# Optimization experiments

Hardware: AMD Instinct MI355X
Metric: run time of the kernel (lower is better)

The kernel has to match this reference:

```python
import jax, jax.numpy as jnp
import numpy as np
from math import sqrt

KERNEL = 25
INV_SQRT2 = 1.0 / sqrt(2.0)


def _moving_avg(xt):
    # xt: [B, L]; replicate-pad then average-pool k=25 stride=1 -> [B, L]
    pad_l = (KERNEL - 1) // 2
    pad_r = KERNEL - 1 - pad_l
    xp = jnp.pad(xt, ((0, 0), (pad_l, pad_r)), mode='edge')[:, None, :]  # [B,1,Lp]
    k = jnp.full((1, 1, KERNEL), 1.0 / KERNEL, dtype=xt.dtype)  # [O,I,W]
    out = jax.lax.conv_general_dilated(xp, k, window_strides=(1,), padding='VALID',
                                       dimension_numbers=('NCH', 'OIH', 'NCH'))
    return out[:, 0, :]


def setup_inputs() -> dict:
    key = jax.random.key(0)
    ks = jax.random.split(key, 7)
    B, L, P, H = 8192, 4096, 720, 2048
    return {
        'x': jax.random.normal(ks[0], (B, L, 1), dtype=jnp.float32),
        'W_trend': jax.random.normal(ks[1], (P, L), dtype=jnp.float32) * 0.02,
        'b_trend': jax.random.normal(ks[2], (P,), dtype=jnp.float32) * 0.02,
        'W_lo': jax.random.normal(ks[3], (P, H), dtype=jnp.float32) * 0.02,
        'b_lo': jax.random.normal(ks[4], (P,), dtype=jnp.float32) * 0.02,
        'W_hi': jax.random.normal(ks[5], (P, H), dtype=jnp.float32) * 0.02,
        'b_hi': jax.random.normal(ks[6], (P,), dtype=jnp.float32) * 0.02,
    }


def reference(x, W_trend, b_trend, W_lo, b_lo, W_hi, b_hi):
    xt = x[..., 0]                              # [B, L]
    trend = _moving_avg(xt)                     # [B, L]
    res = xt - trend                            # [B, L]
    res_mean = jnp.mean(res, axis=-1, keepdims=True)
    # torch.std is unbiased (ddof=1)
    res_std = jnp.std(res, axis=-1, keepdims=True, ddof=1) + 1e-5
    res_norm = (res - res_mean) / res_std       # [B, L]
    # Haar DWT (stride-2 conv with [1,1]/sqrt2 and [1,-1]/sqrt2); L even -> no pad
    even, odd = res_norm[:, 0::2], res_norm[:, 1::2]  # [B, L/2]
    res_lo = (even + odd) * INV_SQRT2
    res_hi = (even - odd) * INV_SQRT2
    pred_trend = trend @ W_trend.T + b_trend    # [B, P]
    pred_res = (res_lo @ W_lo.T + b_lo) + (res_hi @ W_hi.T + b_hi)
    total = pred_trend + pred_res * res_std     # res_std broadcasts [B,1]
    return total[..., None]                     # [B, P, 1]
```

## Files before the change

kernel.cpp:

```cpp
#include <hip/hip_runtime.h>

typedef unsigned short u16;
typedef unsigned int   u32;
typedef __attribute__((ext_vector_type(8))) short bf16x8;
typedef __attribute__((ext_vector_type(4))) float f32x4;

#define LROW 4096
#define NB   8192
#define PCOL 720
#define NPAD 768
#define HH   2048
#define INV_SQRT2F 0.70710678118654752440f

#define WS_XBF_BYTES ((size_t)67108864)
#define WS_G_BYTES   ((size_t)6291456)
#define WS_MIN       (WS_XBF_BYTES + WS_G_BYTES + (size_t)NB * 4)

__device__ __forceinline__ u16 f2bf(float f) {
    union { float f; u32 u; } v; v.f = f;
    u32 r = v.u + 0x7FFFu + ((v.u >> 16) & 1u);
    return (u16)(r >> 16);
}

#define SWZ(i) ((i) ^ (((i) >> 5) & 31))

__global__ __launch_bounds__(256) void prep_rows(const float* __restrict__ x,
                                                 u16* __restrict__ xbf,
                                                 float* __restrict__ stdv) {
    __shared__ float S[LROW];
    __shared__ float wred[4];
    __shared__ float ends[2];
    __shared__ float rred[8];
    const int tid = threadIdx.x;
    const int lane = tid & 63, wv = tid >> 6;
    const size_t b = blockIdx.x;

    const float4* xr4 = (const float4*)(x + b * LROW);
    float4 q0 = xr4[tid * 4 + 0], q1 = xr4[tid * 4 + 1];
    float4 q2 = xr4[tid * 4 + 2], q3 = xr4[tid * 4 + 3];
    float r[16];
    r[0]=q0.x; r[1]=q0.y; r[2]=q0.z; r[3]=q0.w;
    r[4]=q1.x; r[5]=q1.y; r[6]=q1.z; r[7]=q1.w;
    r[8]=q2.x; r[9]=q2.y; r[10]=q2.z; r[11]=q2.w;
    r[12]=q3.x; r[13]=q3.y; r[14]=q3.z; r[15]=q3.w;

    float ps[16];
    float a = 0.f;
    #pragma unroll
    for (int k = 0; k < 16; ++k) { a += r[k]; ps[k] = a; }
    const float segsum = a;

    float v = segsum;
    #pragma unroll
    for (int off = 1; off < 64; off <<= 1) {
        float o = __shfl_up(v, off);
        if (lane >= off) v += o;
    }
    if (lane == 63) wred[wv] = v;
    if (tid == 0)   ends[0] = r[0];
    if (tid == 255) ends[1] = r[15];
    __syncthreads();

    float wbase = 0.f;
    #pragma unroll
    for (int w = 0; w < 4; ++w) if (w < wv) wbase += wred[w];
    const float ebase = wbase + v - segsum;

    #pragma unroll
    for (int k = 0; k < 16; ++k) {
        const int i = (tid << 4) + k;
        S[SWZ(i)] = ebase + ps[k];
    }
    __syncthreads();

    const float x0 = ends[0], xl = ends[1];
    float s1 = 0.f, s2 = 0.f;
    u16 ob[16];
    #pragma unroll
    for (int k = 0; k < 16; ++k) {
        const int i = (tid << 4) + k;
        int h = i + 12; h = h > LROW - 1 ? LROW - 1 : h;
        float wsum = S[SWZ(h)];
        if (i >= 13) wsum -= S[SWZ(i - 13)];
        if (i < 12) wsum += (float)(12 - i) * x0;
        if (i > LROW - 13) wsum += (float)(i - (LROW - 13)) * xl;
        const float xi = r[k];
        const float rr = xi - wsum * 0.04f;
        s1 += rr; s2 += rr * rr;
        ob[k] = f2bf(xi);
    }

    uint4 o0, o1;
    o0.x = (u32)ob[0]  | ((u32)ob[1]  << 16);
    o0.y = (u32)ob[2]  | ((u32)ob[3]  << 16);
    o0.z = (u32)ob[4]  | ((u32)ob[5]  << 16);
    o0.w = (u32)ob[6]  | ((u32)ob[7]  << 16);
    o1.x = (u32)ob[8]  | ((u32)ob[9]  << 16);
    o1.y = (u32)ob[10] | ((u32)ob[11] << 16);
    o1.z = (u32)ob[12] | ((u32)ob[13] << 16);
    o1.w = (u32)ob[14] | ((u32)ob[15] << 16);
    uint4* op = (uint4*)(xbf + b * LROW + ((size_t)tid << 4));
    op[0] = o0; op[1] = o1;

    #pragma unroll
    for (int off = 32; off; off >>= 1) {
        s1 += __shfl_down(s1, off);
        s2 += __shfl_down(s2, off);
    }
    if (lane == 0) { rred[wv * 2] = s1; rred[wv * 2 + 1] = s2; }
    __syncthreads();
    if (tid == 0) {
        const float S1 = rred[0] + rred[2] + rred[4] + rred[6];
        const float S2 = rred[1] + rred[3] + rred[5] + rred[7];
        const float mean = S1 / (float)LROW;
        float var = (S2 - (float)LROW * mean * mean) / (float)(LROW - 1);
        var = var < 0.f ? 0.f : var;
        stdv[b] = sqrtf(var) + 1e-5f;
    }
}

__global__ __launch_bounds__(256) void prep_weights(const float* __restrict__ Wt,
                                                    const float* __restrict__ Wlo,
                                                    const float* __restrict__ Whi,
                                                    u16* __restrict__ Gm) {
    __shared__ float S[LROW];
    __shared__ float wred[4];
    __shared__ float sred[4];
    const int tid = threadIdx.x;
    const int lane = tid & 63, wv = tid >> 6;
    const int p = blockIdx.x;
    u16* grow = Gm + (size_t)p * LROW;
    if (p >= PCOL) {
        uint4 z; z.x = z.y = z.z = z.w = 0u;
        uint4* g4 = (uint4*)grow;
        for (int i = tid; i < LROW / 8; i += 256) g4[i] = z;
        return;
    }
    const float4* wt4 = (const float4*)(Wt + (size_t)p * LROW);
    float4 q0 = wt4[tid * 4 + 0], q1 = wt4[tid * 4 + 1];
    float4 q2 = wt4[tid * 4 + 2], q3 = wt4[tid * 4 + 3];
    const float4* lo4 = (const float4*)(Wlo + (size_t)p * HH);
    const float4* hi4 = (const float4*)(Whi + (size_t)p * HH);
    float4 a0 = lo4[tid * 2 + 0], a1 = lo4[tid * 2 + 1];
    float4 b0 = hi4[tid * 2 + 0], b1 = hi4[tid * 2 + 1];

    float w[16];
    w[0]=q0.x; w[1]=q0.y; w[2]=q0.z; w[3]=q0.w;
    w[4]=q1.x; w[5]=q1.y; w[6]=q1.z; w[7]=q1.w;
    w[8]=q2.x; w[9]=q2.y; w[10]=q2.z; w[11]=q2.w;
    w[12]=q3.x; w[13]=q3.y; w[14]=q3.z; w[15]=q3.w;
    float lv[8] = {a0.x,a0.y,a0.z,a0.w,a1.x,a1.y,a1.z,a1.w};
    float hv[8] = {b0.x,b0.y,b0.z,b0.w,b1.x,b1.y,b1.z,b1.w};

    float u[16], z_[16];
    float slo = 0.f;
    #pragma unroll
    for (int j = 0; j < 8; ++j) {
        u[2*j]   = (lv[j] + hv[j]) * INV_SQRT2F;
        u[2*j+1] = (lv[j] - hv[j]) * INV_SQRT2F;
        slo += lv[j];
    }
    #pragma unroll
    for (int k = 0; k < 16; ++k) z_[k] = w[k] - u[k];

    float ps[16];
    float a = 0.f;
    #pragma unroll
    for (int k = 0; k < 16; ++k) { a += z_[k]; ps[k] = a; }
    const float segsum = a;

    float v = segsum;
    #pragma unroll
    for (int off = 1; off < 64; off <<= 1) {
        float o = __shfl_up(v, off);
        if (lane >= off) v += o;
    }
    if (lane == 63) wred[wv] = v;
    #pragma unroll
    for (int off = 32; off; off >>= 1) slo += __shfl_down(slo, off);
    if (lane == 0) sred[wv] = slo;
    __syncthreads();

    float wbase = 0.f;
    #pragma unroll
    for (int ww = 0; ww < 4; ++ww) if (ww < wv) wbase += wred[ww];
    const float ebase = wbase + v - segsum;
    const float SLO = sred[0] + sred[1] + sred[2] + sred[3];

    #pragma unroll
    for (int k = 0; k < 16; ++k) {
        const int i = (tid << 4) + k;
        S[SWZ(i)] = ebase + ps[k];
    }
    __syncthreads();

    const float coef = -1.4142135623730951f * SLO / (float)LROW;
    u16 ob[16];
    #pragma unroll
    for (int k = 0; k < 16; ++k) {
        const int l = (tid << 4) + k;
        float zT;
        if (l == 0) {
            float acc = 0.f;
            for (int m = 0; m <= 12; ++m) acc += S[SWZ(m)];
            zT = acc * 0.04f;
        } else if (l == LROW - 1) {
            float acc = 0.f;
            for (int m = 0; m <= 12; ++m) acc += S[SWZ(LROW - 2 - m)];
            zT = (13.f * S[SWZ(LROW - 1)] - acc) * 0.04f;
        } else {
            int h = l + 12; h = h > LROW - 1 ? LROW - 1 : h;
            float t_ = S[SWZ(h)];
            if (l >= 13) t_ -= S[SWZ(l - 13)];
            zT = t_ * 0.04f;
        }
        float c;
        const int dmin = l < (LROW - 1 - l) ? l : (LROW - 1 - l);
        if (dmin >= 12)      c = 0.f;
        else if (dmin == 0)  c = -66.f / 25.f;
        else                 c = (float)(12 - dmin) * 0.04f;
        ob[k] = f2bf(zT + u[k] + coef * c);
    }

    uint4 o0, o1;
    o0.x = (u32)ob[0]  | ((u32)ob[1]  << 16);
    o0.y = (u32)ob[2]  | ((u32)ob[3]  << 16);
    o0.z = (u32)ob[4]  | ((u32)ob[5]  << 16);
    o0.w = (u32)ob[6]  | ((u32)ob[7]  << 16);
    o1.x = (u32)ob[8]  | ((u32)ob[9]  << 16);
    o1.y = (u32)ob[10] | ((u32)ob[11] << 16);
    o1.z = (u32)ob[12] | ((u32)ob[13] << 16);
    o1.w = (u32)ob[14] | ((u32)ob[15] << 16);
    uint4* op = (uint4*)(grow + ((size_t)tid << 4));
    op[0] = o0; op[1] = o1;
}

typedef __attribute__((address_space(1))) void gvoid;
typedef __attribute__((address_space(3))) void lvoid;
#define GLD16(g, l_) __builtin_amdgcn_global_load_lds((gvoid*)(g), (lvoid*)(l_), 16, 0, 0)
#define MF(a, b, c) __builtin_amdgcn_mfma_f32_16x16x32_bf16(a, b, c, 0, 0, 0)

#define ABUF 16384
#define BBASE 49152
#define BBUF 12288

#define STAGE_A2(T, DB) do { \
    char* d_ = Sm + (DB) * ABUF; \
    const size_t go_ = (size_t)((T) + 2) * 128; \
    GLD16(s0 + go_, d_ + dof0); GLD16(s1 + go_, d_ + dof1); \
    GLD16(s2 + go_, d_ + dof2); GLD16(s3 + go_, d_ + dof3); \
} while (0)

#define STAGE_B1(T, DB) do { \
    char* d_ = Sm + BBASE + (DB) * BBUF; \
    const size_t go_ = (size_t)((T) + 1) * 128; \
    GLD16(s0 + go_, d_ + dof0); GLD16(s1 + go_, d_ + dof1); GLD16(s2 + go_, d_ + dof2); \
} while (0)

#define ITER(T, RA, RB, SAB, SBB, VA, VB, SA, SB) do { \
    if (isA) { asm volatile("s_waitcnt vmcnt(" #VA ")" ::: "memory"); } \
    else     { asm volatile("s_waitcnt vmcnt(" #VB ")" ::: "memory"); } \
    __builtin_amdgcn_s_barrier(); \
    __builtin_amdgcn_sched_barrier(0); \
    if (isA) { if (SA) STAGE_A2(T, SAB); } \
    else     { if (SB) STAGE_B1(T, SBB); } \
    __builtin_amdgcn_sched_barrier(0); \
    const char* ab_ = Sm + (RA) * ABUF + aro; \
    const char* bb_ = Sm + BBASE + (RB) * BBUF + bro; \
    bf16x8 a0_ = *(const bf16x8*)(ab_); \
    bf16x8 a1_ = *(const bf16x8*)(ab_ + 2048); \
    bf16x8 a2_ = *(const bf16x8*)(ab_ + 4096); \
    bf16x8 a3_ = *(const bf16x8*)(ab_ + 6144); \
    bf16x8 b0_ = *(const bf16x8*)(bb_); \
    bf16x8 b1_ = *(const bf16x8*)(bb_ + 2048); \
    bf16x8 b2_ = *(const bf16x8*)(bb_ + 4096); \
    asm volatile("s_waitcnt lgkmcnt(0)" ::: "memory"); \
    __builtin_amdgcn_sched_barrier(0); \
    __builtin_amdgcn_s_setprio(1); \
    acc[0][0]=MF(a0_,b0_,acc[0][0]); acc[0][1]=MF(a0_,b1_,acc[0][1]); acc[0][2]=MF(a0_,b2_,acc[0][2]); \
    acc[1][0]=MF(a1_,b0_,acc[1][0]); acc[1][1]=MF(a1_,b1_,acc[1][1]); acc[1][2]=MF(a1_,b2_,acc[1][2]); \
    acc[2][0]=MF(a2_,b0_,acc[2][0]); acc[2][1]=MF(a2_,b1_,acc[2][1]); acc[2][2]=MF(a2_,b2_,acc[2][2]); \
    acc[3][0]=MF(a3_,b0_,acc[3][0]); acc[3][1]=MF(a3_,b1_,acc[3][1]); acc[3][2]=MF(a3_,b2_,acc[3][2]); \
    __builtin_amdgcn_s_setprio(0); \
} while (0)

__global__ __launch_bounds__(512, 4) void gemm_fused(const u16* __restrict__ Abf,
                                                     const u16* __restrict__ Gbf,
                                                     const float* __restrict__ bt,
                                                     const float* __restrict__ bl,
                                                     const float* __restrict__ bh,
                                                     const float* __restrict__ stdv,
                                                     float* __restrict__ out) {
    __shared__ __align__(16) char Sm[73728];
    const int tid = threadIdx.x;
    const int l = tid & 63, wid = tid >> 6;
    const int kp = wid & 1, wm = (wid >> 1) & 1, wn = wid >> 2;
    const bool isA = (wid < 4);

    const int orig = blockIdx.x;
    const int chunk = orig & 7, pos = orig >> 3;
    const int bx = pos & 7;
    const int by = (chunk << 3) + (pos >> 3);
    const int m0 = by * 128;
    const int n0 = bx * 96;

    const int sgb = (((l & 7) ^ (l >> 3)) << 4);
    const char* s0; const char* s1; const char* s2; const char* s3;
    int dof0, dof1, dof2, dof3;
    if (isA) {
        const int r0 = wid * 32;
        s0 = (const char*)Abf + ((size_t)(m0 + r0 +  0 + (l >> 3)) << 13) + sgb;
        s1 = (const char*)Abf + ((size_t)(m0 + r0 +  8 + (l >> 3)) << 13) + sgb;
        s2 = (const char*)Abf + ((size_t)(m0 + r0 + 16 + (l >> 3)) << 13) + sgb;
        s3 = (const char*)Abf + ((size_t)(m0 + r0 + 24 + (l >> 3)) << 13) + sgb;
        dof0 = r0 * 128; dof1 = dof0 + 1024; dof2 = dof0 + 2048; dof3 = dof0 + 3072;
    } else {
        const int r0 = (wid - 4) * 24;
        s0 = (const char*)Gbf + ((size_t)(n0 + r0 +  0 + (l >> 3)) << 13) + sgb;
        s1 = (const char*)Gbf + ((size_t)(n0 + r0 +  8 + (l >> 3)) << 13) + sgb;
        s2 = (const char*)Gbf + ((size_t)(n0 + r0 + 16 + (l >> 3)) << 13) + sgb;
        s3 = s0;
        dof0 = r0 * 128; dof1 = dof0 + 1024; dof2 = dof0 + 2048; dof3 = dof0;
    }

    const int slot = ((kp << 2) + (l >> 4)) ^ (l & 7);
    const int aro = (wm * 64 + (l & 15)) * 128 + (slot << 4);
    const int bro = (wn * 48 + (l & 15)) * 128 + (slot << 4);

    f32x4 acc[4][3] = {};

    if (isA) {
        GLD16(s0, Sm + dof0); GLD16(s1, Sm + dof1);
        GLD16(s2, Sm + dof2); GLD16(s3, Sm + dof3);
        GLD16(s0 + 128, Sm + ABUF + dof0); GLD16(s1 + 128, Sm + ABUF + dof1);
        GLD16(s2 + 128, Sm + ABUF + dof2); GLD16(s3 + 128, Sm + ABUF + dof3);
    } else {
        GLD16(s0, Sm + BBASE + dof0); GLD16(s1, Sm + BBASE + dof1);
        GLD16(s2, Sm + BBASE + dof2);
    }

    for (int t = 0; t < 60; t += 6) {
        ITER(t + 0, 0, 0, 2, 1, 4, 0, 1, 1);
        ITER(t + 1, 1, 1, 0, 0, 4, 0, 1, 1);
        ITER(t + 2, 2, 0, 1, 1, 4, 0, 1, 1);
        ITER(t + 3, 0, 1, 2, 0, 4, 0, 1, 1);
        ITER(t + 4, 1, 0, 0, 1, 4, 0, 1, 1);
        ITER(t + 5, 2, 1, 1, 0, 4, 0, 1, 1);
    }
    ITER(60, 0, 0, 2, 1, 4, 0, 1, 1);
    ITER(61, 1, 1, 0, 0, 4, 0, 1, 1);
    ITER(62, 2, 0, 1, 1, 4, 0, 0, 1);
    ITER(63, 0, 1, 2, 0, 0, 0, 0, 0);

    __syncthreads();
    float* red = (float*)Sm;
    const int pb_ = (wm * 2 + wn) * 3264;
    const int rr_ = (l >> 4) << 2;
    const int cc_ = l & 15;
    if (kp == 1) {
        #pragma unroll
        for (int m = 0; m < 4; ++m)
            #pragma unroll
            for (int n = 0; n < 3; ++n)
                *(f32x4*)(red + pb_ + (n * 16 + cc_) * 68 + m * 16 + rr_) = acc[m][n];
    }
    __syncthreads();
    if (kp == 0) {
        const int crow = m0 + wm * 64 + rr_;
        const int ccol = n0 + wn * 48 + cc_;
        float btv[3], bsv[3];
        #pragma unroll
        for (int n = 0; n < 3; ++n) {
            const int col = ccol + n * 16;
            if (col < PCOL) { btv[n] = bt[col]; bsv[n] = bl[col] + bh[col]; }
            else            { btv[n] = 0.f; bsv[n] = 0.f; }
        }
        #pragma unroll
        for (int m = 0; m < 4; ++m) {
            const int row = crow + m * 16;
            const float4 sv = *(const float4*)(stdv + row);
            #pragma unroll
            for (int n = 0; n < 3; ++n) {
                const int col = ccol + n * 16;
                if (col < PCOL) {
                    const f32x4 pv = *(const f32x4*)(red + pb_ + (n * 16 + cc_) * 68 + m * 16 + rr_);
                    float* orow = out + (size_t)row * PCOL + col;
                    #pragma unroll
                    for (int j = 0; j < 4; ++j) {
                        const float s = (j == 0) ? sv.x : (j == 1) ? sv.y : (j == 2) ? sv.z : sv.w;
                        orow[(size_t)j * PCOL] = acc[m][n][j] + pv[j] + btv[n] + s * bsv[n];
                    }
                }
            }
        }
    }
}

extern "C" void kernel_launch(void* const* d_in, const int* in_sizes, int n_in,
                              void* d_out, int out_size, void* d_ws, size_t ws_size,
                              hipStream_t stream) {
    (void)in_sizes; (void)n_in; (void)out_size;
    if (ws_size < WS_MIN) return;

    const float* x  = (const float*)d_in[0];
    const float* Wt = (const float*)d_in[1];
    const float* bt = (const float*)d_in[2];
    const float* Wl = (const float*)d_in[3];
    const float* bl = (const float*)d_in[4];
    const float* Wh = (const float*)d_in[5];
    const float* bh = (const float*)d_in[6];
    float* out = (float*)d_out;

    char* ws = (char*)d_ws;
    u16*   xbf = (u16*)ws;
    u16*   Gm  = (u16*)(ws + WS_XBF_BYTES);
    float* sd  = (float*)(ws + WS_XBF_BYTES + WS_G_BYTES);

    prep_rows<<<NB, 256, 0, stream>>>(x, xbf, sd);
    prep_weights<<<NPAD, 256, 0, stream>>>(Wt, Wl, Wh, Gm);
    gemm_fused<<<512, 512, 0, stream>>>(xbf, Gm, bt, bl, bh, sd, out);
}
```

Baseline: 100.2 us.

## Load GEMM B operand directly into registers, stage only A through LDS

```diff
diff --git a/kernel.cpp b/kernel.cpp
--- a/kernel.cpp
+++ b/kernel.cpp
@@ -239,48 +239,42 @@
 typedef __attribute__((address_space(3))) void lvoid;
 #define GLD16(g, l_) __builtin_amdgcn_global_load_lds((gvoid*)(g), (lvoid*)(l_), 16, 0, 0)
 #define MF(a, b, c) __builtin_amdgcn_mfma_f32_16x16x32_bf16(a, b, c, 0, 0, 0)
+#define GL16(dst, p) asm volatile("global_load_dwordx4 %0, %1, off" : "=&v"(dst) : "v"(p) : "memory")
 
 #define ABUF 16384
-#define BBASE 49152
-#define BBUF 12288
-
-#define STAGE_A2(T, DB) do { \
-    char* d_ = Sm + (DB) * ABUF; \
-    const size_t go_ = (size_t)((T) + 2) * 128; \
-    GLD16(s0 + go_, d_ + dof0); GLD16(s1 + go_, d_ + dof1); \
-    GLD16(s2 + go_, d_ + dof2); GLD16(s3 + go_, d_ + dof3); \
+
+#define STAGE_A(T, DB) do { \
+    char* d_ = Sm + (DB) * ABUF + wid * 2048; \
+    const size_t go_ = (size_t)(T) * 128; \
+    GLD16(sA0 + go_, d_); \
+    GLD16(sA1 + go_, d_ + 1024); \
 } while (0)
 
-#define STAGE_B1(T, DB) do { \
-    char* d_ = Sm + BBASE + (DB) * BBUF; \
-    const size_t go_ = (size_t)((T) + 1) * 128; \
-    GLD16(s0 + go_, d_ + dof0); GLD16(s1 + go_, d_ + dof1); GLD16(s2 + go_, d_ + dof2); \
-} while (0)
-
-#define ITER(T, RA, RB, SAB, SBB, VA, VB, SA, SB) do { \
-    if (isA) { asm volatile("s_waitcnt vmcnt(" #VA ")" ::: "memory"); } \
-    else     { asm volatile("s_waitcnt vmcnt(" #VB ")" ::: "memory"); } \
+#define ITER(T, AR, SAB, C0, C1, C2, N0, N1, N2, V1, V2, SA, SB) do { \
+    asm volatile("s_waitcnt vmcnt(" #V1 ")" ::: "memory"); \
     __builtin_amdgcn_s_barrier(); \
     __builtin_amdgcn_sched_barrier(0); \
-    if (isA) { if (SA) STAGE_A2(T, SAB); } \
-    else     { if (SB) STAGE_B1(T, SBB); } \
+    if (SA) STAGE_A((T) + 2, SAB); \
+    if (SB) { \
+        const size_t go_ = (size_t)((T) + 1) * 128; \
+        GL16(N0, pb0 + go_); \
+        GL16(N1, pb1 + go_); \
+        GL16(N2, pb2 + go_); \
+    } \
+    asm volatile("s_waitcnt vmcnt(" #V2 ")" ::: "memory"); \
     __builtin_amdgcn_sched_barrier(0); \
-    const char* ab_ = Sm + (RA) * ABUF + aro; \
-    const char* bb_ = Sm + BBASE + (RB) * BBUF + bro; \
+    const char* ab_ = Sm + (AR) * ABUF + aro; \
     bf16x8 a0_ = *(const bf16x8*)(ab_); \
     bf16x8 a1_ = *(const bf16x8*)(ab_ + 2048); \
     bf16x8 a2_ = *(const bf16x8*)(ab_ + 4096); \
     bf16x8 a3_ = *(const bf16x8*)(ab_ + 6144); \
-    bf16x8 b0_ = *(const bf16x8*)(bb_); \
-    bf16x8 b1_ = *(const bf16x8*)(bb_ + 2048); \
-    bf16x8 b2_ = *(const bf16x8*)(bb_ + 4096); \
     asm volatile("s_waitcnt lgkmcnt(0)" ::: "memory"); \
     __builtin_amdgcn_sched_barrier(0); \
     __builtin_amdgcn_s_setprio(1); \
-    acc[0][0]=MF(a0_,b0_,acc[0][0]); acc[0][1]=MF(a0_,b1_,acc[0][1]); acc[0][2]=MF(a0_,b2_,acc[0][2]); \
-    acc[1][0]=MF(a1_,b0_,acc[1][0]); acc[1][1]=MF(a1_,b1_,acc[1][1]); acc[1][2]=MF(a1_,b2_,acc[1][2]); \
-    acc[2][0]=MF(a2_,b0_,acc[2][0]); acc[2][1]=MF(a2_,b1_,acc[2][1]); acc[2][2]=MF(a2_,b2_,acc[2][2]); \
-    acc[3][0]=MF(a3_,b0_,acc[3][0]); acc[3][1]=MF(a3_,b1_,acc[3][1]); acc[3][2]=MF(a3_,b2_,acc[3][2]); \
+    acc[0][0]=MF(a0_,C0,acc[0][0]); acc[0][1]=MF(a0_,C1,acc[0][1]); acc[0][2]=MF(a0_,C2,acc[0][2]); \
+    acc[1][0]=MF(a1_,C0,acc[1][0]); acc[1][1]=MF(a1_,C1,acc[1][1]); acc[1][2]=MF(a1_,C2,acc[1][2]); \
+    acc[2][0]=MF(a2_,C0,acc[2][0]); acc[2][1]=MF(a2_,C1,acc[2][1]); acc[2][2]=MF(a2_,C2,acc[2][2]); \
+    acc[3][0]=MF(a3_,C0,acc[3][0]); acc[3][1]=MF(a3_,C1,acc[3][1]); acc[3][2]=MF(a3_,C2,acc[3][2]); \
     __builtin_amdgcn_s_setprio(0); \
 } while (0)
 
@@ -291,11 +285,10 @@
                                                      const float* __restrict__ bh,
                                                      const float* __restrict__ stdv,
                                                      float* __restrict__ out) {
-    __shared__ __align__(16) char Sm[73728];
+    __shared__ __align__(16) char Sm[53248];
     const int tid = threadIdx.x;
     const int l = tid & 63, wid = tid >> 6;
     const int kp = wid & 1, wm = (wid >> 1) & 1, wn = wid >> 2;
-    const bool isA = (wid < 4);
 
     const int orig = blockIdx.x;
     const int chunk = orig & 7, pos = orig >> 3;
@@ -305,52 +298,35 @@
     const int n0 = bx * 96;
 
     const int sgb = (((l & 7) ^ (l >> 3)) << 4);
-    const char* s0; const char* s1; const char* s2; const char* s3;
-    int dof0, dof1, dof2, dof3;
-    if (isA) {
-        const int r0 = wid * 32;
-        s0 = (const char*)Abf + ((size_t)(m0 + r0 +  0 + (l >> 3)) << 13) + sgb;
-        s1 = (const char*)Abf + ((size_t)(m0 + r0 +  8 + (l >> 3)) << 13) + sgb;
-        s2 = (const char*)Abf + ((size_t)(m0 + r0 + 16 + (l >> 3)) << 13) + sgb;
-        s3 = (const char*)Abf + ((size_t)(m0 + r0 + 24 + (l >> 3)) << 13) + sgb;
-        dof0 = r0 * 128; dof1 = dof0 + 1024; dof2 = dof0 + 2048; dof3 = dof0 + 3072;
-    } else {
-        const int r0 = (wid - 4) * 24;
-        s0 = (const char*)Gbf + ((size_t)(n0 + r0 +  0 + (l >> 3)) << 13) + sgb;
-        s1 = (const char*)Gbf + ((size_t)(n0 + r0 +  8 + (l >> 3)) << 13) + sgb;
-        s2 = (const char*)Gbf + ((size_t)(n0 + r0 + 16 + (l >> 3)) << 13) + sgb;
-        s3 = s0;
-        dof0 = r0 * 128; dof1 = dof0 + 1024; dof2 = dof0 + 2048; dof3 = dof0;
-    }
+    const char* sA0 = (const char*)Abf + ((size_t)(m0 + wid * 16 + (l >> 3)) << 13) + sgb;
+    const char* sA1 = (const char*)Abf + ((size_t)(m0 + wid * 16 + 8 + (l >> 3)) << 13) + sgb;
 
     const int slot = ((kp << 2) + (l >> 4)) ^ (l & 7);
     const int aro = (wm * 64 + (l & 15)) * 128 + (slot << 4);
-    const int bro = (wn * 48 + (l & 15)) * 128 + (slot << 4);
+
+    const char* pb0 = (const char*)Gbf + ((size_t)(n0 + wn * 48 +  0 + (l & 15)) << 13) + kp * 64 + ((l >> 4) << 4);
+    const char* pb1 = (const char*)Gbf + ((size_t)(n0 + wn * 48 + 16 + (l & 15)) << 13) + kp * 64 + ((l >> 4) << 4);
+    const char* pb2 = (const char*)Gbf + ((size_t)(n0 + wn * 48 + 32 + (l & 15)) << 13) + kp * 64 + ((l >> 4) << 4);
 
     f32x4 acc[4][3] = {};
-
-    if (isA) {
-        GLD16(s0, Sm + dof0); GLD16(s1, Sm + dof1);
-        GLD16(s2, Sm + dof2); GLD16(s3, Sm + dof3);
-        GLD16(s0 + 128, Sm + ABUF + dof0); GLD16(s1 + 128, Sm + ABUF + dof1);
-        GLD16(s2 + 128, Sm + ABUF + dof2); GLD16(s3 + 128, Sm + ABUF + dof3);
-    } else {
-        GLD16(s0, Sm + BBASE + dof0); GLD16(s1, Sm + BBASE + dof1);
-        GLD16(s2, Sm + BBASE + dof2);
-    }
+    bf16x8 B00, B01, B02, B10, B11, B12;
+
+    STAGE_A(0, 0);
+    STAGE_A(1, 1);
+    GL16(B00, pb0); GL16(B01, pb1); GL16(B02, pb2);
 
     for (int t = 0; t < 60; t += 6) {
-        ITER(t + 0, 0, 0, 2, 1, 4, 0, 1, 1);
-        ITER(t + 1, 1, 1, 0, 0, 4, 0, 1, 1);
-        ITER(t + 2, 2, 0, 1, 1, 4, 0, 1, 1);
-        ITER(t + 3, 0, 1, 2, 0, 4, 0, 1, 1);
-        ITER(t + 4, 1, 0, 0, 1, 4, 0, 1, 1);
-        ITER(t + 5, 2, 1, 1, 0, 4, 0, 1, 1);
-    }
-    ITER(60, 0, 0, 2, 1, 4, 0, 1, 1);
-    ITER(61, 1, 1, 0, 0, 4, 0, 1, 1);
-    ITER(62, 2, 0, 1, 1, 4, 0, 0, 1);
-    ITER(63, 0, 1, 2, 0, 0, 0, 0, 0);
+        ITER(t + 0, 0, 2, B00, B01, B02, B10, B11, B12, 5, 5, 1, 1);
+        ITER(t + 1, 1, 0, B10, B11, B12, B00, B01, B02, 5, 5, 1, 1);
+        ITER(t + 2, 2, 1, B00, B01, B02, B10, B11, B12, 5, 5, 1, 1);
+        ITER(t + 3, 0, 2, B10, B11, B12, B00, B01, B02, 5, 5, 1, 1);
+        ITER(t + 4, 1, 0, B00, B01, B02, B10, B11, B12, 5, 5, 1, 1);
+        ITER(t + 5, 2, 1, B10, B11, B12, B00, B01, B02, 5, 5, 1, 1);
+    }
+    ITER(60, 0, 2, B00, B01, B02, B10, B11, B12, 5, 5, 1, 1);
+    ITER(61, 1, 0, B10, B11, B12, B00, B01, B02, 5, 5, 1, 1);
+    ITER(62, 2, 0, B00, B01, B02, B10, B11, B12, 5, 3, 0, 1);
+    ITER(63, 0, 0, B10, B11, B12, B00, B01, B02, 3, 0, 0, 0);
 
     __syncthreads();
     float* red = (float*)Sm;
```

New measurement: 148.8 us. 48.5% more time.
